# Performance work log

Hardware: AMD Instinct MI355X
Metric: run time of the kernel (lower is better)

The kernel has to match this reference:

```python
import jax, jax.numpy as jnp
import numpy as np
from jax import lax

B, S, H = 2, 2048, 768
FF = 1536
E = 8
TOP_K = 2


def setup_inputs() -> dict:
    key = jax.random.key(0)
    k1, k2, k3, k4 = jax.random.split(key, 4)
    hidden_states = jax.random.normal(k1, (B, S, H), dtype=jnp.float32)
    # torch init: weight.normal_() for experts; nn.Linear default init for gate (approx normal here is fine for a numerics baseline)
    gate_w = jax.random.normal(k2, (E, H), dtype=jnp.float32) * 0.02
    w_fc = jax.random.normal(k3, (E, FF, H), dtype=jnp.float32) * 0.02
    w_proj = jax.random.normal(k4, (E, H, FF), dtype=jnp.float32) * 0.02
    return {"hidden_states": hidden_states, "gate_w": gate_w, "w_fc": w_fc, "w_proj": w_proj}


def reference(hidden_states, gate_w, w_fc, w_proj):
    b, s, h = hidden_states.shape
    x = hidden_states.reshape(-1, h)                      # [T, H]
    # --- top-k gating (logits in float32, as in the torch code) ---
    logits = (x @ gate_w.T).astype(jnp.float32)           # [T, E]
    top_logits, top_idx = lax.top_k(logits, TOP_K)        # [T, K]
    gates = jax.nn.softmax(top_logits, axis=1).astype(x.dtype)  # [T, K]
    # combined per-token/per-expert gate: g[t,e] = sum_k gates[t,k]*[idx[t,k]==e]
    onehot = jax.nn.one_hot(top_idx, E, dtype=x.dtype)    # [T, K, E]
    g = jnp.einsum('tk,tke->te', gates, onehot)           # [T, E]
    # --- experts: gather + per-expert GEMM + gated scatter-add combine ---
    # Equivalent math: tokens with zero gate for expert e contribute nothing,
    # so compute each expert on all tokens and weight by g[:, e].
    out = jnp.zeros_like(x)
    for e in range(E):  # fixed small loop over experts (structurally distinct weights)
        hmid = jax.nn.gelu(x @ w_fc[e].T, approximate=False)   # [T, FF] (torch gelu = erf form)
        out = out + g[:, e:e + 1] * (hmid @ w_proj[e].T)       # [T, H]
    out = out.reshape(b, s, h)
    return out, logits
```

## Files before the change

### kernel.cpp

```cpp
#include <hip/hip_runtime.h>
#include <hip/hip_bf16.h>
#include <math.h>
#include <stdint.h>

#define TOKENS 4096
#define HDIM   768
#define FFDIM  1536
#define NEXP   8
#define NCTA   24
#define NCTB   12
#define GEMM_GRID 768

typedef __attribute__((ext_vector_type(8))) short bf16x8;
typedef __attribute__((ext_vector_type(4))) float f32x4;

__device__ __forceinline__ unsigned short f2bf(float f) {
    union { float f; uint32_t u; } c; c.f = f;
    uint32_t u = c.u;
    uint32_t r = (u + 0x7FFFu + ((u >> 16) & 1u)) >> 16;
    return (unsigned short)r;
}

__device__ __forceinline__ void gload_lds16(const void* g, void* l) {
    __builtin_amdgcn_global_load_lds(
        (const __attribute__((address_space(1))) void*)g,
        (__attribute__((address_space(3))) void*)l, 16, 0, 0);
}

__device__ __forceinline__ void wave_vmem_drain() {
    __builtin_amdgcn_s_waitcnt(0x0F70);
    asm volatile("" ::: "memory");
}

__global__ void cast_bf16_2(const float* __restrict__ s1, unsigned short* __restrict__ d1,
                            const float* __restrict__ s2, unsigned short* __restrict__ d2,
                            int n4) {
    int stride = gridDim.x * blockDim.x;
    for (int i = blockIdx.x * blockDim.x + threadIdx.x; i < 2 * n4; i += stride) {
        const float4* s = (i < n4) ? (const float4*)s1 : (const float4*)s2;
        ushort4* d = (i < n4) ? (ushort4*)d1 : (ushort4*)d2;
        int j = (i < n4) ? i : i - n4;
        float4 v = s[j];
        ushort4 o;
        o.x = f2bf(v.x); o.y = f2bf(v.y); o.z = f2bf(v.z); o.w = f2bf(v.w);
        d[j] = o;
    }
}

__global__ __launch_bounds__(256) void gating(
    const float* __restrict__ x, const float* __restrict__ gw,
    float* __restrict__ logits,
    int* __restrict__ tok_e, float* __restrict__ tok_g,
    unsigned short* __restrict__ x_bf, float* __restrict__ outp)
{
    float4 zz = make_float4(0.f, 0.f, 0.f, 0.f);
#pragma unroll
    for (int j = 0; j < 3; j++)
        ((float4*)outp)[blockIdx.x * 768 + j * 256 + threadIdx.x] = zz;

    int t = blockIdx.x * 4 + (threadIdx.x >> 6);
    int lane = threadIdx.x & 63;
    const float4* xt = (const float4*)(x + (size_t)t * HDIM);
    const float4* gw4 = (const float4*)gw;
    ushort4* xbt = (ushort4*)(x_bf + (size_t)t * HDIM);
    float acc[NEXP];
#pragma unroll
    for (int e = 0; e < NEXP; e++) acc[e] = 0.f;
#pragma unroll
    for (int it = 0; it < 3; it++) {
        int i = lane + it * 64;
        float4 xv = xt[i];
        ushort4 o;
        o.x = f2bf(xv.x); o.y = f2bf(xv.y); o.z = f2bf(xv.z); o.w = f2bf(xv.w);
        xbt[i] = o;
#pragma unroll
        for (int e = 0; e < NEXP; e++) {
            float4 wv = gw4[e * 192 + i];
            acc[e] += xv.x * wv.x + xv.y * wv.y + xv.z * wv.z + xv.w * wv.w;
        }
    }
#pragma unroll
    for (int e = 0; e < NEXP; e++) {
#pragma unroll
        for (int off = 32; off > 0; off >>= 1)
            acc[e] += __shfl_xor(acc[e], off);
    }
    if (lane == 0) {
        float4 l0 = make_float4(acc[0], acc[1], acc[2], acc[3]);
        float4 l1 = make_float4(acc[4], acc[5], acc[6], acc[7]);
        float4* lp = (float4*)(logits + (size_t)t * NEXP);
        lp[0] = l0; lp[1] = l1;
        int i0 = 0; float v0 = acc[0];
#pragma unroll
        for (int e = 1; e < NEXP; e++) if (acc[e] > v0) { v0 = acc[e]; i0 = e; }
        int i1 = -1; float v1 = -3.4e38f;
#pragma unroll
        for (int e = 0; e < NEXP; e++) if (e != i0 && acc[e] > v1) { v1 = acc[e]; i1 = e; }
        float g0 = 1.f / (1.f + expf(v1 - v0));
        tok_e[t * 2] = i0; tok_e[t * 2 + 1] = i1;
        tok_g[t * 2] = g0; tok_g[t * 2 + 1] = 1.f - g0;
    }
}

__global__ __launch_bounds__(1024) void build_lists(
    const int* __restrict__ tok_e, const float* __restrict__ tok_g,
    int* __restrict__ counts, int* __restrict__ bases,
    int* __restrict__ fillA, int* __restrict__ fillB,
    int* __restrict__ workA, int* __restrict__ workB,
    int* __restrict__ entries, float* __restrict__ gates)
{
    __shared__ unsigned long long wlo[16], whi[16];
    __shared__ int scnt[8];
    int tid = threadIdx.x;
    int lane = tid & 63, wid = tid >> 6;

    int eL[8]; float gL[8];
    int4 ea = ((const int4*)tok_e)[tid * 2];
    int4 eb = ((const int4*)tok_e)[tid * 2 + 1];
    float4 ga = ((const float4*)tok_g)[tid * 2];
    float4 gb = ((const float4*)tok_g)[tid * 2 + 1];
    eL[0] = ea.x; eL[1] = ea.y; eL[2] = ea.z; eL[3] = ea.w;
    eL[4] = eb.x; eL[5] = eb.y; eL[6] = eb.z; eL[7] = eb.w;
    gL[0] = ga.x; gL[1] = ga.y; gL[2] = ga.z; gL[3] = ga.w;
    gL[4] = gb.x; gL[5] = gb.y; gL[6] = gb.z; gL[7] = gb.w;

    unsigned long long clo = 0, chi = 0;
#pragma unroll
    for (int j = 0; j < 8; j++) {
        int e = eL[j];
        unsigned long long one = 1ull << ((e & 3) * 16);
        if (e < 4) clo += one; else chi += one;
    }
    unsigned long long ilo = clo, ihi = chi;
#pragma unroll
    for (int s = 1; s < 64; s <<= 1) {
        unsigned long long t1 = __shfl_up(ilo, s);
        unsigned long long t2 = __shfl_up(ihi, s);
        if (lane >= s) { ilo += t1; ihi += t2; }
    }
    if (lane == 63) { wlo[wid] = ilo; whi[wid] = ihi; }
    __syncthreads();
    if (tid == 0) {
        unsigned long long rl = 0, rh = 0;
#pragma unroll
        for (int i = 0; i < 16; i++) {
            unsigned long long a = wlo[i], b = whi[i];
            wlo[i] = rl; whi[i] = rh;
            rl += a; rh += b;
        }
        int c[8];
#pragma unroll
        for (int e = 0; e < 4; e++) {
            c[e]     = (int)((rl >> (e * 16)) & 0xFFFF);
            c[e + 4] = (int)((rh >> (e * 16)) & 0xFFFF);
        }
        int b = 0;
#pragma unroll
        for (int e = 0; e < NEXP; e++) {
            scnt[e] = c[e]; counts[e] = c[e]; bases[e] = b; b += c[e];
            int rts = (c[e] + 63) >> 6;
            fillA[e] = rts * NCTA;
            fillB[e] = rts * NCTB;
        }
    }
    __syncthreads();
    if (tid < NEXP * NCTA) {
        int e = tid / NCTA, ct = tid % NCTA;
        int rts = (scnt[e] + 63) >> 6;
        for (int r = 0; r < rts; r++)
            workA[(ct * rts + r) * 8 + e] = (ct << 20) | (e << 16) | (r << 6);
    }
    if (tid >= 256 && tid < 256 + NEXP * NCTB) {
        int t2 = tid - 256;
        int e = t2 / NCTB, ct = t2 % NCTB;
        int rts = (scnt[e] + 63) >> 6;
        for (int r = 0; r < rts; r++)
            workB[(ct * rts + r) * 8 + e] = (ct << 20) | (e << 16) | (r << 6);
    }
    unsigned long long rlo = wlo[wid] + (ilo - clo);
    unsigned long long rhi = whi[wid] + (ihi - chi);
#pragma unroll
    for (int j = 0; j < 8; j++) {
        int e = eL[j];
        int sh = (e & 3) * 16;
        unsigned long long one = 1ull << sh;
        int slot;
        if (e < 4) { slot = (int)((rlo >> sh) & 0xFFFF); rlo += one; }
        else       { slot = (int)((rhi >> sh) & 0xFFFF); rhi += one; }
        entries[e * TOKENS + slot] = tid * 8 + j;
        gates[e * TOKENS + slot]   = gL[j];
    }
}

template<int KD, int ND, bool IS_FC>
__global__ __launch_bounds__(256, 3) void moe_gemm(
    const unsigned short* __restrict__ Asrc,
    const unsigned short* __restrict__ Bsrc,
    const int* __restrict__ counts,
    const int* __restrict__ bases,
    const int* __restrict__ fill,
    const int* __restrict__ work,
    const int* __restrict__ entries,
    const float* __restrict__ gates,
    unsigned short* __restrict__ hmid,
    float* __restrict__ outp)
{
    int bkt = blockIdx.x & 7;
    int nfill = fill[bkt];

    int tid = threadIdx.x;
    int w = tid >> 6;
    int l = tid & 63;
    int p4  = l & 3;
    int lr16 = l >> 2;
    int lo = l & 15;
    int q  = l >> 4;

    __shared__ __align__(16) unsigned short sA[4 * 64 * 32];
    __shared__ __align__(16) unsigned short sB[4 * 64 * 32];
    unsigned short* sAq = sA + w * 2048;
    unsigned short* sBq = sB + w * 2048;

    int aOff[4], bOff[4];
#pragma unroll
    for (int i = 0; i < 4; i++) {
        int m = i * 16 + lo;
        aOff[i] = m * 32 + (q ^ ((m >> 1) & 3)) * 8;
        bOff[i] = aOff[i];
    }

    for (int p = (blockIdx.x >> 3) * 4 + w; p < nfill; p += (GEMM_GRID / 8) * 4) {
        int pk   = work[p * 8 + bkt];
        int ct   = pk >> 20;
        int e    = (pk >> 16) & 0xF;
        int row0 = pk & 0xFFFF;
        int n_e  = counts[e];
        int ebase = bases[e];
        int n0 = ct * 64;
        const int* lst = entries + e * TOKENS;

        const unsigned short* Ag[4];
        const unsigned short* Bg[4];
#pragma unroll
        for (int c = 0; c < 4; c++) {
            int rr = c * 16 + lr16;
            int gr = row0 + rr;
            int id = gr < n_e ? gr : n_e - 1;
            size_t arow = IS_FC ? (size_t)(lst[id] >> 1) : (size_t)(ebase + id);
            int gseg = p4 ^ ((rr >> 1) & 3);
            Ag[c] = Asrc + arow * KD + gseg * 8;
            Bg[c] = Bsrc + ((size_t)e * ND + n0 + rr) * KD + gseg * 8;
        }

        f32x4 acc[4][4];
#pragma unroll
        for (int i = 0; i < 4; i++)
#pragma unroll
            for (int j = 0; j < 4; j++) acc[i][j] = (f32x4){0.f, 0.f, 0.f, 0.f};

        for (int k0 = 0; k0 < KD; k0 += 32) {
#pragma unroll
            for (int c = 0; c < 4; c++) gload_lds16(Ag[c] + k0, sAq + c * 512);
#pragma unroll
            for (int c = 0; c < 4; c++) gload_lds16(Bg[c] + k0, sBq + c * 512);
            wave_vmem_drain();
            bf16x8 a[4], b[4];
#pragma unroll
            for (int i = 0; i < 4; i++) a[i] = *(const bf16x8*)(sAq + aOff[i]);
#pragma unroll
            for (int j = 0; j < 4; j++) b[j] = *(const bf16x8*)(sBq + bOff[j]);
#pragma unroll
            for (int i = 0; i < 4; i++)
#pragma unroll
                for (int j = 0; j < 4; j++)
                    acc[i][j] = __builtin_amdgcn_mfma_f32_16x16x32_bf16(a[i], b[j], acc[i][j], 0, 0, 0);
        }

#pragma unroll
        for (int i = 0; i < 4; i++) {
            int rowB = row0 + i * 16 + q * 4;
#pragma unroll
            for (int rr = 0; rr < 4; rr++) {
                int orow = rowB + rr;
                if (orow < n_e) {
                    if (IS_FC) {
                        size_t hrow = (size_t)(ebase + orow);
#pragma unroll
                        for (int j = 0; j < 4; j++) {
                            float v = acc[i][j][rr];
                            v = 0.5f * v * (1.f + erff(v * 0.70710678118654752f));
                            hmid[hrow * ND + n0 + j * 16 + lo] = f2bf(v);
                        }
                    } else {
                        int token = lst[orow] >> 1;
                        float g = gates[e * TOKENS + orow];
#pragma unroll
                        for (int j = 0; j < 4; j++) {
                            atomicAdd(&outp[(size_t)token * ND + n0 + j * 16 + lo],
                                      acc[i][j][rr] * g);
                        }
                    }
                }
            }
        }
    }
}

extern "C" void kernel_launch(void* const* d_in, const int* in_sizes, int n_in,
                              void* d_out, int out_size, void* d_ws, size_t ws_size,
                              hipStream_t stream) {
    const float* x     = (const float*)d_in[0];
    const float* gw    = (const float*)d_in[1];
    const float* wfc   = (const float*)d_in[2];
    const float* wproj = (const float*)d_in[3];
    float* outp   = (float*)d_out;
    float* logits = outp + (size_t)TOKENS * HDIM;

    char* ws = (char*)d_ws;
    int*   counts  = (int*)ws;
    int*   bases   = (int*)(ws + 64);
    int*   fillA   = (int*)(ws + 128);
    int*   fillB   = (int*)(ws + 192);
    int*   workA   = (int*)(ws + 256);
    size_t off = 256 + (size_t)3072 * 8 * 4;
    int*   workB   = (int*)(ws + off); off += (size_t)1536 * 8 * 4;
    int*   entries = (int*)(ws + off);
    float* gates   = (float*)(ws + off + NEXP * TOKENS * 4);
    off += 2ull * NEXP * TOKENS * 4;
    int*   tok_e   = (int*)(ws + off);   off += (size_t)TOKENS * 2 * 4;
    float* tok_g   = (float*)(ws + off); off += (size_t)TOKENS * 2 * 4;
    unsigned short* x_bf   = (unsigned short*)(ws + off); off += (size_t)TOKENS * HDIM * 2;
    unsigned short* wfc_bf = (unsigned short*)(ws + off); off += (size_t)NEXP * FFDIM * HDIM * 2;
    unsigned short* wpj_bf = (unsigned short*)(ws + off); off += (size_t)NEXP * HDIM * FFDIM * 2;
    unsigned short* hmid   = (unsigned short*)(ws + off);

    cast_bf16_2<<<2048, 256, 0, stream>>>(wfc, wfc_bf, wproj, wpj_bf,
                                          NEXP * FFDIM * HDIM / 4);
    gating<<<TOKENS / 4, 256, 0, stream>>>(x, gw, logits, tok_e, tok_g, x_bf, outp);
    build_lists<<<1, 1024, 0, stream>>>(tok_e, tok_g, counts, bases, fillA, fillB,
                                        workA, workB, entries, gates);
    moe_gemm<HDIM, FFDIM, true ><<<GEMM_GRID, 256, 0, stream>>>(
        x_bf, wfc_bf, counts, bases, fillA, workA, entries, gates, hmid, outp);
    moe_gemm<FFDIM, HDIM, false><<<GEMM_GRID, 256, 0, stream>>>(
        hmid, wpj_bf, counts, bases, fillB, workB, entries, gates, hmid, outp);
}
```

Baseline: 243.6 us.

## Switch MoE GEMMs to shared 256x128 block tiles with split-K for projection

Replaces the per-wave independent 64x64 tiles with a 512-thread block computing a 256x128 tile shared in LDS, with K steps of 64 and block-level barriers. This raises operand reuse across waves and cuts redundant global loads of weights and activations. The second GEMM also splits K in two halves, relying on the existing atomic accumulation, to keep enough work items with the larger tiles. The risks are lower occupancy, barrier stalls with no double buffering, and padding waste when experts have few tokens.

```diff
diff --git a/kernel.cpp b/kernel.cpp
--- a/kernel.cpp
+++ b/kernel.cpp
@@ -7,9 +7,9 @@
 #define HDIM   768
 #define FFDIM  1536
 #define NEXP   8
-#define NCTA   24
-#define NCTB   12
-#define GEMM_GRID 768
+#define NCT1   12
+#define NCT2   6
+#define GEMM_GRID 512
 
 typedef __attribute__((ext_vector_type(8))) short bf16x8;
 typedef __attribute__((ext_vector_type(4))) float f32x4;
@@ -25,11 +25,6 @@
     __builtin_amdgcn_global_load_lds(
         (const __attribute__((address_space(1))) void*)g,
         (__attribute__((address_space(3))) void*)l, 16, 0, 0);
-}
-
-__device__ __forceinline__ void wave_vmem_drain() {
-    __builtin_amdgcn_s_waitcnt(0x0F70);
-    asm volatile("" ::: "memory");
 }
 
 __global__ void cast_bf16_2(const float* __restrict__ s1, unsigned short* __restrict__ d1,
@@ -158,24 +153,27 @@
 #pragma unroll
         for (int e = 0; e < NEXP; e++) {
             scnt[e] = c[e]; counts[e] = c[e]; bases[e] = b; b += c[e];
-            int rts = (c[e] + 63) >> 6;
-            fillA[e] = rts * NCTA;
-            fillB[e] = rts * NCTB;
+            int rts = (c[e] + 255) >> 8;
+            fillA[e] = rts * NCT1;
+            fillB[e] = rts * NCT2 * 2;
         }
     }
     __syncthreads();
-    if (tid < NEXP * NCTA) {
-        int e = tid / NCTA, ct = tid % NCTA;
-        int rts = (scnt[e] + 63) >> 6;
+    if (tid < NEXP * NCT1) {
+        int e = tid / NCT1, ct = tid % NCT1;
+        int rts = (scnt[e] + 255) >> 8;
         for (int r = 0; r < rts; r++)
-            workA[(ct * rts + r) * 8 + e] = (ct << 20) | (e << 16) | (r << 6);
-    }
-    if (tid >= 256 && tid < 256 + NEXP * NCTB) {
+            workA[(ct * rts + r) * 8 + e] = (ct << 24) | (e << 20) | (r << 8);
+    }
+    if (tid >= 256 && tid < 256 + NEXP * NCT2 * 2) {
         int t2 = tid - 256;
-        int e = t2 / NCTB, ct = t2 % NCTB;
-        int rts = (scnt[e] + 63) >> 6;
+        int e = t2 / (NCT2 * 2);
+        int rem = t2 % (NCT2 * 2);
+        int ct = rem >> 1, kh = rem & 1;
+        int rts = (scnt[e] + 255) >> 8;
         for (int r = 0; r < rts; r++)
-            workB[(ct * rts + r) * 8 + e] = (ct << 20) | (e << 16) | (r << 6);
+            workB[((ct * 2 + kh) * rts + r) * 8 + e] =
+                (ct << 24) | (e << 20) | (kh << 19) | (r << 8);
     }
     unsigned long long rlo = wlo[wid] + (ilo - clo);
     unsigned long long rhi = whi[wid] + (ihi - chi);
@@ -192,8 +190,8 @@
     }
 }
 
-template<int KD, int ND, bool IS_FC>
-__global__ __launch_bounds__(256, 3) void moe_gemm(
+template<int KD, int ND, int KSPLIT, bool IS_FC>
+__global__ __launch_bounds__(512, 4) void moe_gemm(
     const unsigned short* __restrict__ Asrc,
     const unsigned short* __restrict__ Bsrc,
     const int* __restrict__ counts,
@@ -211,45 +209,54 @@
     int tid = threadIdx.x;
     int w = tid >> 6;
     int l = tid & 63;
-    int p4  = l & 3;
-    int lr16 = l >> 2;
+    int sg  = l & 7;
+    int lr8 = l >> 3;
     int lo = l & 15;
     int q  = l >> 4;
-
-    __shared__ __align__(16) unsigned short sA[4 * 64 * 32];
-    __shared__ __align__(16) unsigned short sB[4 * 64 * 32];
-    unsigned short* sAq = sA + w * 2048;
-    unsigned short* sBq = sB + w * 2048;
-
-    int aOff[4], bOff[4];
+    int wr = w >> 1, wc = w & 1;
+
+    __shared__ __align__(16) unsigned short sA[256 * 64];
+    __shared__ __align__(16) unsigned short sB[128 * 64];
+
+    int aOff[4][2], bOff[4][2];
 #pragma unroll
     for (int i = 0; i < 4; i++) {
-        int m = i * 16 + lo;
-        aOff[i] = m * 32 + (q ^ ((m >> 1) & 3)) * 8;
-        bOff[i] = aOff[i];
-    }
-
-    for (int p = (blockIdx.x >> 3) * 4 + w; p < nfill; p += (GEMM_GRID / 8) * 4) {
+        int m = wr * 64 + i * 16 + lo;
+        int n = wc * 64 + i * 16 + lo;
+#pragma unroll
+        for (int s = 0; s < 2; s++) {
+            aOff[i][s] = m * 64 + ((s * 4 + q) ^ (m & 7)) * 8;
+            bOff[i][s] = n * 64 + ((s * 4 + q) ^ (n & 7)) * 8;
+        }
+    }
+
+    for (int p = blockIdx.x >> 3; p < nfill; p += GEMM_GRID / 8) {
         int pk   = work[p * 8 + bkt];
-        int ct   = pk >> 20;
-        int e    = (pk >> 16) & 0xF;
-        int row0 = pk & 0xFFFF;
+        int ct   = pk >> 24;
+        int e    = (pk >> 20) & 0xF;
+        int kh   = (pk >> 19) & 1;
+        int row0 = pk & 0x3FFF;
         int n_e  = counts[e];
         int ebase = bases[e];
-        int n0 = ct * 64;
+        int n0 = ct * 128;
         const int* lst = entries + e * TOKENS;
 
-        const unsigned short* Ag[4];
-        const unsigned short* Bg[4];
+        const unsigned short* Ag[4]; int aLds[4];
 #pragma unroll
         for (int c = 0; c < 4; c++) {
-            int rr = c * 16 + lr16;
+            int rr = w * 32 + c * 8 + lr8;
             int gr = row0 + rr;
             int id = gr < n_e ? gr : n_e - 1;
             size_t arow = IS_FC ? (size_t)(lst[id] >> 1) : (size_t)(ebase + id);
-            int gseg = p4 ^ ((rr >> 1) & 3);
-            Ag[c] = Asrc + arow * KD + gseg * 8;
-            Bg[c] = Bsrc + ((size_t)e * ND + n0 + rr) * KD + gseg * 8;
+            Ag[c] = Asrc + arow * KD + (size_t)((sg ^ (rr & 7)) * 8);
+            aLds[c] = (w * 32 + c * 8) * 64;
+        }
+        const unsigned short* Bg[2]; int bLds[2];
+#pragma unroll
+        for (int c = 0; c < 2; c++) {
+            int rr = w * 16 + c * 8 + lr8;
+            Bg[c] = Bsrc + ((size_t)e * ND + n0 + rr) * KD + (size_t)((sg ^ (rr & 7)) * 8);
+            bLds[c] = (w * 16 + c * 8) * 64;
         }
 
         f32x4 acc[4][4];
@@ -258,27 +265,33 @@
 #pragma unroll
             for (int j = 0; j < 4; j++) acc[i][j] = (f32x4){0.f, 0.f, 0.f, 0.f};
 
-        for (int k0 = 0; k0 < KD; k0 += 32) {
-#pragma unroll
-            for (int c = 0; c < 4; c++) gload_lds16(Ag[c] + k0, sAq + c * 512);
-#pragma unroll
-            for (int c = 0; c < 4; c++) gload_lds16(Bg[c] + k0, sBq + c * 512);
-            wave_vmem_drain();
-            bf16x8 a[4], b[4];
-#pragma unroll
-            for (int i = 0; i < 4; i++) a[i] = *(const bf16x8*)(sAq + aOff[i]);
-#pragma unroll
-            for (int j = 0; j < 4; j++) b[j] = *(const bf16x8*)(sBq + bOff[j]);
-#pragma unroll
-            for (int i = 0; i < 4; i++)
-#pragma unroll
-                for (int j = 0; j < 4; j++)
-                    acc[i][j] = __builtin_amdgcn_mfma_f32_16x16x32_bf16(a[i], b[j], acc[i][j], 0, 0, 0);
+        const int kBeg = kh * (KD / KSPLIT);
+        const int kEnd = kBeg + KD / KSPLIT;
+        for (int k0 = kBeg; k0 < kEnd; k0 += 64) {
+#pragma unroll
+            for (int c = 0; c < 4; c++) gload_lds16(Ag[c] + k0, sA + aLds[c]);
+#pragma unroll
+            for (int c = 0; c < 2; c++) gload_lds16(Bg[c] + k0, sB + bLds[c]);
+            __syncthreads();
+#pragma unroll
+            for (int s = 0; s < 2; s++) {
+                bf16x8 a[4], b[4];
+#pragma unroll
+                for (int i = 0; i < 4; i++) a[i] = *(const bf16x8*)(sA + aOff[i][s]);
+#pragma unroll
+                for (int j = 0; j < 4; j++) b[j] = *(const bf16x8*)(sB + bOff[j][s]);
+#pragma unroll
+                for (int i = 0; i < 4; i++)
+#pragma unroll
+                    for (int j = 0; j < 4; j++)
+                        acc[i][j] = __builtin_amdgcn_mfma_f32_16x16x32_bf16(a[i], b[j], acc[i][j], 0, 0, 0);
+            }
+            __syncthreads();
         }
 
 #pragma unroll
         for (int i = 0; i < 4; i++) {
-            int rowB = row0 + i * 16 + q * 4;
+            int rowB = row0 + wr * 64 + i * 16 + q * 4;
 #pragma unroll
             for (int rr = 0; rr < 4; rr++) {
                 int orow = rowB + rr;
@@ -289,14 +302,14 @@
                         for (int j = 0; j < 4; j++) {
                             float v = acc[i][j][rr];
                             v = 0.5f * v * (1.f + erff(v * 0.70710678118654752f));
-                            hmid[hrow * ND + n0 + j * 16 + lo] = f2bf(v);
+                            hmid[hrow * ND + n0 + wc * 64 + j * 16 + lo] = f2bf(v);
                         }
                     } else {
                         int token = lst[orow] >> 1;
                         float g = gates[e * TOKENS + orow];
 #pragma unroll
                         for (int j = 0; j < 4; j++) {
-                            atomicAdd(&outp[(size_t)token * ND + n0 + j * 16 + lo],
+                            atomicAdd(&outp[(size_t)token * ND + n0 + wc * 64 + j * 16 + lo],
                                       acc[i][j][rr] * g);
                         }
                     }
@@ -322,8 +335,8 @@
     int*   fillA   = (int*)(ws + 128);
     int*   fillB   = (int*)(ws + 192);
     int*   workA   = (int*)(ws + 256);
-    size_t off = 256 + (size_t)3072 * 8 * 4;
-    int*   workB   = (int*)(ws + off); off += (size_t)1536 * 8 * 4;
+    size_t off = 256 + (size_t)512 * 8 * 4;
+    int*   workB   = (int*)(ws + off); off += (size_t)512 * 8 * 4;
     int*   entries = (int*)(ws + off);
     float* gates   = (float*)(ws + off + NEXP * TOKENS * 4);
     off += 2ull * NEXP * TOKENS * 4;
@@ -339,8 +352,8 @@
     gating<<<TOKENS / 4, 256, 0, stream>>>(x, gw, logits, tok_e, tok_g, x_bf, outp);
     build_lists<<<1, 1024, 0, stream>>>(tok_e, tok_g, counts, bases, fillA, fillB,
                                         workA, workB, entries, gates);
-    moe_gemm<HDIM, FFDIM, true ><<<GEMM_GRID, 256, 0, stream>>>(
+    moe_gemm<HDIM, FFDIM, 1, true ><<<GEMM_GRID, 512, 0, stream>>>(
         x_bf, wfc_bf, counts, bases, fillA, workA, entries, gates, hmid, outp);
-    moe_gemm<FFDIM, HDIM, false><<<GEMM_GRID, 256, 0, stream>>>(
+    moe_gemm<FFDIM, HDIM, 2, false><<<GEMM_GRID, 512, 0, stream>>>(
         hmid, wpj_bf, counts, bases, fillB, workB, entries, gates, hmid, outp);
 }
```

Result: no change. 246.7 us (+1.3%).
